# Performance work log

Hardware: AMD Instinct MI355X
Metric: run time of the kernel (lower is better)

## Reference

```python
import jax, jax.numpy as jnp
import numpy as np

R_S, R_C, P, L, NVOX, CH = 48, 144, 27, 2, 128, 128


def encode(x, L=L):
    # NeRF-style positional encoding: [sin(2^l x), cos(2^l x)] for l in range(L)
    feats = []
    for l in range(L):
        f = (2.0 ** l) * x
        feats.append(jnp.sin(f))
        feats.append(jnp.cos(f))
    return jnp.concatenate(feats, axis=-1)


def setup_inputs() -> dict:
    key = jax.random.key(0)
    ks = jax.random.split(key, 8)
    Np = 524288
    xyz = jax.random.uniform(ks[0], (Np, 3), dtype=jnp.float32)          # inside bbox [0,1]^3
    directions = jax.random.normal(ks[1], (Np, 3), dtype=jnp.float32)
    # voxel grid buffer: linspace over bbox per axis -> (3, NVOX)
    voxel = jnp.stack([jnp.linspace(0.0, 1.0, NVOX)] * 3, axis=0).astype(jnp.float32)
    sigma = 0.1 * jax.random.normal(ks[2], (3, R_S, NVOX), dtype=jnp.float32)
    feature = 0.1 * jax.random.normal(ks[3], (3, R_C, NVOX), dtype=jnp.float32)
    B = jax.random.normal(ks[4], (R_C, P), dtype=jnp.float32)
    din = (P + 3) * L * 2  # 120
    W1 = jax.random.normal(ks[5], (din, CH), dtype=jnp.float32) / jnp.sqrt(din)
    b1 = jnp.zeros((CH,), jnp.float32)
    W2 = jax.random.normal(ks[6], (CH, CH), dtype=jnp.float32) / jnp.sqrt(CH)
    b2 = jnp.zeros((CH,), jnp.float32)
    W3 = jax.random.normal(ks[7], (CH, 3), dtype=jnp.float32) / jnp.sqrt(CH)
    b3 = jnp.zeros((3,), jnp.float32)
    return {"xyz": xyz, "directions": directions, "voxel": voxel, "sigma": sigma,
            "feature": feature, "B": B, "W1": W1, "b1": b1, "W2": W2, "b2": b2,
            "W3": W3, "b3": b3}


def reference(xyz, directions, voxel, sigma, feature, B, W1, b1, W2, b2, W3, b3):
    SIGMA_BIAS = -5.0
    x = xyz.T  # (3, Np)
    Nv = voxel.shape[1]
    # snap_to_voxels: per-axis searchsorted + clamp + gather of grid coords
    inds = jax.vmap(jnp.searchsorted)(voxel, x)           # (3, Np)
    il = jnp.clip(inds - 1, 0, Nv - 1)
    ir = jnp.clip(inds, 0, Nv - 1)
    vl = jnp.take_along_axis(voxel, il, axis=1)           # (3, Np)
    vr = jnp.take_along_axis(voxel, ir, axis=1)
    w = (x - vl) / (vr - vl + 1e-6)                       # (3, Np) lerp weights

    # density: gather (3,R_s,Np), lerp, prod over axes(xyz), sum over rank
    sl = jnp.take_along_axis(sigma, il[:, None, :], axis=2)
    sr = jnp.take_along_axis(sigma, ir[:, None, :], axis=2)
    s = sl + (sr - sl) * w[:, None, :]                    # (3, R_s, Np)
    sigmas = jnp.sum(jnp.prod(s, axis=0), axis=0)         # (Np,)
    sigmas = jax.nn.softplus(sigmas + SIGMA_BIAS)

    # features: same pattern on (3,R_c,Np), then small matmul with B
    fl = jnp.take_along_axis(feature, il[:, None, :], axis=2)
    fr = jnp.take_along_axis(feature, ir[:, None, :], axis=2)
    f = fl + (fr - fl) * w[:, None, :]                    # (3, R_c, Np)
    feats = jnp.einsum('rn,rp->np', jnp.prod(f, axis=0), B)  # (Np, P)

    h = jnp.concatenate([encode(feats, L), encode(directions, L)], axis=1)  # (Np, 120)
    h = jax.nn.leaky_relu(h @ W1 + b1, negative_slope=0.01)
    h = jax.nn.leaky_relu(h @ W2 + b2, negative_slope=0.01)
    rgb = jax.nn.sigmoid(h @ W3 + b3)                     # (Np, 3)
    return sigmas, rgb
```

## Files before the change

kernel.cpp:

```cpp
#include <hip/hip_runtime.h>
#include <cstdint>

constexpr int RS  = 48;
constexpr int RC  = 144;
constexpr int PP  = 27;
constexpr int NV  = 128;
constexpr int CHN = 128;

constexpr int SIG_D  = 3 * NV * 64;
constexpr int FEAT_D = 3 * NV * 160;
constexpr int NPAIR  = SIG_D + FEAT_D;
constexpr int FR_B  = 0;
constexpr int FR_W1 = 5120;
constexpr int FR_W2 = 21504;
constexpr int FR_W3 = 37888;
constexpr int FR_B2 = 39936;
constexpr int FR_TOT = 45056;

typedef __attribute__((ext_vector_type(8))) short short8;
typedef __attribute__((ext_vector_type(4))) float f32x4;
typedef __attribute__((ext_vector_type(2))) unsigned int u32x2;
typedef __attribute__((ext_vector_type(4))) unsigned int u32x4;
typedef _Float16 h2 __attribute__((ext_vector_type(2)));

__device__ __forceinline__ short f2bf(float f) {
    unsigned int u = __builtin_bit_cast(unsigned int, f);
    u += 0x7fffu + ((u >> 16) & 1u);
    return (short)(u >> 16);
}
__device__ __forceinline__ unsigned int pk2bf(float a, float b) {
    unsigned short ua = __builtin_bit_cast(unsigned short, (__bf16)a);
    unsigned short ub = __builtin_bit_cast(unsigned short, (__bf16)b);
    return (unsigned int)ua | ((unsigned int)ub << 16);
}
__device__ __forceinline__ float bflo(unsigned int u) { return __builtin_bit_cast(float, u << 16); }
__device__ __forceinline__ float bfhi(unsigned int u) { return __builtin_bit_cast(float, u & 0xffff0000u); }
__device__ __forceinline__ float dot2lerp(unsigned int lodelta, h2 wv) {
#if __has_builtin(__builtin_amdgcn_fdot2)
    return __builtin_amdgcn_fdot2(__builtin_bit_cast(h2, lodelta), wv, 0.f, false);
#else
    h2 a = __builtin_bit_cast(h2, lodelta);
    return (float)a.x * (float)wv.x + (float)a.y * (float)wv.y;
#endif
}

#define GLO(dst, base, OFF) \
    asm volatile("global_load_dwordx4 %0, %1, off offset:" OFF : "=&v"(dst) : "v"(base))
#define WAITV(N) do { asm volatile("s_waitcnt vmcnt(" #N ")" ::: "memory"); \
                      __builtin_amdgcn_sched_barrier(0); } while (0)
#define ISSUE_FK(buf, O1, O2) do { \
    GLO(buf[0], fb0, O1); GLO(buf[1], fb0, O2); \
    GLO(buf[2], fb1, O1); GLO(buf[3], fb1, O2); \
    GLO(buf[4], fb2, O1); GLO(buf[5], fb2, O2); } while (0)

__global__ void prep_tables(const float* __restrict__ sigma, const float* __restrict__ feature,
                            unsigned int* __restrict__ wt) {
    int idx = blockIdx.x * 256 + threadIdx.x;
    if (idx >= NPAIR) return;
    float lo = 0.f, hi = 0.f;
    if (idx < SIG_D) {
        int a = idx / 8192, t = idx % 8192;
        int v = t / 64, r = t % 64;
        if (r < RS) {
            lo = sigma[(a * RS + r) * NV + v];
            hi = sigma[(a * RS + r) * NV + min(v + 1, NV - 1)];
        }
    } else {
        int j = idx - SIG_D;
        int a = j / 20480, t = j % 20480;
        int v = t / 160, r = t % 160;
        if (r < RC) {
            lo = feature[(a * RC + r) * NV + v];
            hi = feature[(a * RC + r) * NV + min(v + 1, NV - 1)];
        }
    }
    _Float16 lh = (_Float16)lo;
    _Float16 dh = (_Float16)(hi - lo);
    wt[idx] = (unsigned int)__builtin_bit_cast(unsigned short, lh) |
              ((unsigned int)__builtin_bit_cast(unsigned short, dh) << 16);
}

__global__ void prep_frags(const float* __restrict__ Bm, const float* __restrict__ W1,
                           const float* __restrict__ W2, const float* __restrict__ W3,
                           short* __restrict__ fr) {
    int idx = blockIdx.x * 256 + threadIdx.x;
    if (idx >= FR_TOT) return;
    float val = 0.f;
    if (idx < FR_W1) {
        int j = idx - FR_B;
        int frag = j >> 9, li = (j >> 3) & 63, e = j & 7;
        int kt = frag >> 1, nt = frag & 1;
        int k = kt * 32 + (li >> 4) * 8 + e;
        int n = nt * 16 + (li & 15);
        val = (k < RC && n < PP) ? Bm[k * PP + n] : 0.f;
    } else if (idx < FR_W2) {
        int j = idx - FR_W1;
        int frag = j >> 9, li = (j >> 3) & 63, e = j & 7;
        int kt = frag >> 3, nt = frag & 7;
        int kn = kt * 32 + (li >> 4) * 8 + e;
        int n = nt * 16 + (li & 15);
        if (kn < 120) {
            int ko;
            if (kn < 108) { ko = (kn & 3) * PP + (kn >> 2); }
            else { int t2 = kn - 108; ko = 108 + (t2 & 3) * 3 + (t2 >> 2); }
            val = W1[ko * CHN + n];
        }
    } else if (idx < FR_W3) {
        int j = idx - FR_W2;
        int frag = j >> 9, li = (j >> 3) & 63, e = j & 7;
        int kt = frag >> 3, nt = frag & 7;
        int k = kt * 32 + (li >> 4) * 8 + e;
        int n = nt * 16 + (li & 15);
        val = W2[k * CHN + n];
    } else if (idx < FR_B2) {
        int j = idx - FR_W3;
        int frag = j >> 9, li = (j >> 3) & 63, e = j & 7;
        int kt = frag;
        int k = kt * 32 + (li >> 4) * 8 + e;
        int n = li & 15;
        val = (n < 3) ? W3[k * 3 + n] : 0.f;
    } else {
        int j = idx - FR_B2;
        int frag = j >> 9, li = (j >> 3) & 63, e = j & 7;
        int kt = frag >> 1, nt = frag & 1;
        int q = li >> 4;
        int n = nt * 16 + (li & 15);
        int k = -1;
        if (kt < 4) k = kt * 32 + (e < 4 ? 4 * q + e : 16 + 4 * q + (e - 4));
        else if (e < 4) k = 128 + 4 * q + e;
        val = (k >= 0 && k < RC && n < PP) ? Bm[k * PP + n] : 0.f;
    }
    fr[idx] = f2bf(val);
}

__device__ __forceinline__ void lerpregs(u32x4 A, u32x4 Bv, h2 wv, float* pr, bool first) {
#pragma unroll
    for (int d = 0; d < 4; ++d) {
        float s0 = dot2lerp(A[d], wv);
        float s1 = dot2lerp(Bv[d], wv);
        if (first) { pr[d] = s0; pr[4 + d] = s1; }
        else       { pr[d] *= s0; pr[4 + d] *= s1; }
    }
}
__device__ __forceinline__ void lerpf8(const unsigned int* rl, h2 wv, float* pr, bool first) {
    u32x4 A  = *(const u32x4*)rl;
    u32x4 Bv = *(const u32x4*)(rl + 4);
    lerpregs(A, Bv, wv, pr, first);
}

__global__ __launch_bounds__(256, 4)
void phaseA(const float* __restrict__ xyz, const float* __restrict__ dird,
            const float* __restrict__ voxel,
            const unsigned int* __restrict__ wt, const short* __restrict__ fr,
            float* __restrict__ out, unsigned short* __restrict__ X64, int Np) {
    __shared__ float voxs[3 * NV];
    __shared__ short bfrs[5120];

    const int tid = threadIdx.x;
    const int wid = tid >> 6;
    const int lane = tid & 63;
    const int quad = lane >> 4, lane16 = lane & 15;
    const int wavebase = blockIdx.x * 64 + wid * 16;
    const int p = wavebase + lane16;

    for (int i = tid; i < 3 * NV; i += 256) voxs[i] = voxel[i];
    for (int i = tid; i < 640; i += 256)
        ((short8*)bfrs)[i] = ((const short8*)(fr + FR_B2))[i];
    __syncthreads();

    const unsigned int* SIGU  = wt;
    const unsigned int* FEATU = wt + SIG_D;

    int ipb[3]; h2 wv[3];
#pragma unroll
    for (int a = 0; a < 3; ++a) {
        float x = xyz[p * 3 + a];
        int ind = (int)ceilf(x * 127.f);
        ind = min(max(ind, 0), 128);
        while (ind > 0 && voxs[a * NV + ind - 1] >= x) --ind;
        while (ind < 128 && voxs[a * NV + ind] < x) ++ind;
        int il = min(max(ind - 1, 0), 127);
        int ir = min(ind, 127);
        float vl = voxs[a * NV + il], vr = voxs[a * NV + ir];
        float w = (x - vl) / (vr - vl + 1e-6f);
        w = (il == 127) ? 1.f : w;
        ipb[a] = min(il, 126);
        wv[a] = h2{(_Float16)1.0f, (_Float16)w};
    }

    const unsigned int* sb0 = SIGU + (0 * NV + ipb[0]) * 64 + quad * 4;
    const unsigned int* sb1 = SIGU + (1 * NV + ipb[1]) * 64 + quad * 4;
    const unsigned int* sb2 = SIGU + (2 * NV + ipb[2]) * 64 + quad * 4;
    const unsigned int* fb0 = FEATU + (0 * NV + ipb[0]) * 160 + quad * 4;
    const unsigned int* fb1 = FEATU + (1 * NV + ipb[1]) * 160 + quad * 4;
    const unsigned int* fb2 = FEATU + (2 * NV + ipb[2]) * 160 + quad * 4;

    u32x4 S[9];
    GLO(S[0], sb0, "0");   GLO(S[1], sb1, "0");   GLO(S[2], sb2, "0");
    GLO(S[3], sb0, "64");  GLO(S[4], sb1, "64");  GLO(S[5], sb2, "64");
    GLO(S[6], sb0, "128"); GLO(S[7], sb1, "128"); GLO(S[8], sb2, "128");
    u32x4 Fa[6], Fb[6];
    ISSUE_FK(Fa, "0", "64");

    WAITV(6);
    float sig = 0.f;
#pragma unroll
    for (int L = 0; L < 3; ++L)
#pragma unroll
        for (int j = 0; j < 4; ++j)
            sig += dot2lerp(S[3 * L][j], wv[0]) * dot2lerp(S[3 * L + 1][j], wv[1])
                 * dot2lerp(S[3 * L + 2][j], wv[2]);
    sig += __shfl_xor(sig, 16);
    sig += __shfl_xor(sig, 32);

    f32x4 acc0 = {0.f, 0.f, 0.f, 0.f}, acc1 = {0.f, 0.f, 0.f, 0.f};
    auto compute_kt = [&](const u32x4* F, int kt) {
        float pr[8];
#pragma unroll
        for (int j = 0; j < 4; ++j) {
            pr[j]     = dot2lerp(F[0][j], wv[0]) * dot2lerp(F[2][j], wv[1]) * dot2lerp(F[4][j], wv[2]);
            pr[4 + j] = dot2lerp(F[1][j], wv[0]) * dot2lerp(F[3][j], wv[1]) * dot2lerp(F[5][j], wv[2]);
        }
        u32x4 uu;
#pragma unroll
        for (int d = 0; d < 4; ++d) uu[d] = pk2bf(pr[2 * d], pr[2 * d + 1]);
        short8 af = __builtin_bit_cast(short8, uu);
        short8 bf0 = *(const short8*)(bfrs + ((kt * 2 + 0) * 64 + lane) * 8);
        short8 bf1 = *(const short8*)(bfrs + ((kt * 2 + 1) * 64 + lane) * 8);
        acc0 = __builtin_amdgcn_mfma_f32_16x16x32_bf16(af, bf0, acc0, 0, 0, 0);
        acc1 = __builtin_amdgcn_mfma_f32_16x16x32_bf16(af, bf1, acc1, 0, 0, 0);
    };

    ISSUE_FK(Fb, "128", "192");
    WAITV(6); compute_kt(Fa, 0);
    ISSUE_FK(Fa, "256", "320");
    WAITV(6); compute_kt(Fb, 1);
    ISSUE_FK(Fb, "384", "448");
    WAITV(6); compute_kt(Fa, 2);
    GLO(Fa[0], fb0, "512"); GLO(Fa[1], fb1, "512"); GLO(Fa[2], fb2, "512");
    WAITV(3); compute_kt(Fb, 3);
    WAITV(0);
    {
        float pr[8];
#pragma unroll
        for (int j = 0; j < 4; ++j) {
            pr[j] = dot2lerp(Fa[0][j], wv[0]) * dot2lerp(Fa[1][j], wv[1]) * dot2lerp(Fa[2][j], wv[2]);
            pr[4 + j] = 0.f;
        }
        u32x4 uu;
#pragma unroll
        for (int d = 0; d < 4; ++d) uu[d] = pk2bf(pr[2 * d], pr[2 * d + 1]);
        short8 af = __builtin_bit_cast(short8, uu);
        short8 bf0 = *(const short8*)(bfrs + ((4 * 2 + 0) * 64 + lane) * 8);
        short8 bf1 = *(const short8*)(bfrs + ((4 * 2 + 1) * 64 + lane) * 8);
        acc0 = __builtin_amdgcn_mfma_f32_16x16x32_bf16(af, bf0, acc0, 0, 0, 0);
        acc1 = __builtin_amdgcn_mfma_f32_16x16x32_bf16(af, bf1, acc1, 0, 0, 0);
    }

    if (lane < 16) out[p] = log1pf(expf(sig - 5.f));
#pragma unroll
    for (int nt = 0; nt < 2; ++nt) {
        int c = nt * 16 + lane16;
        f32x4 A = nt ? acc1 : acc0;
        if (c < PP) {
#pragma unroll
            for (int j = 0; j < 4; ++j) {
                int prow = wavebase + quad * 4 + j;
                X64[prow * 32 + c] = (unsigned short)__builtin_bit_cast(unsigned short, (__bf16)A[j]);
            }
        }
    }
    if (quad < 3) {
        float d = dird[p * 3 + quad];
        X64[p * 32 + 27 + quad] = (unsigned short)__builtin_bit_cast(unsigned short, (__bf16)d);
    } else {
        *(unsigned int*)(X64 + p * 32 + 30) = 0u;
    }
}

__global__ __launch_bounds__(256, 4)
void phaseB(const unsigned short* __restrict__ X64, const short* __restrict__ fr,
            const float* __restrict__ b1, const float* __restrict__ b2,
            const float* __restrict__ b3, float* __restrict__ out, int Np) {
    __shared__ char T[4 * 32 * 256];
    const int tid = threadIdx.x;
    const int wid = tid >> 6;
    const int lane = tid & 63;
    const int quad = lane >> 4, lane16 = lane & 15;
    const int rowbase = blockIdx.x * 128 + wid * 32;
    char* Tw = T + wid * 32 * 256;

    const short* W1F = fr + FR_W1;
    const short* W2F = fr + FR_W2;
    const short* W3F = fr + FR_W3;

    short8 af[2][4];
#pragma unroll
    for (int mt = 0; mt < 2; ++mt)
#pragma unroll
        for (int kt = 0; kt < 4; ++kt) {
            unsigned int d = *(const unsigned int*)(X64 + (rowbase + mt * 16 + lane16) * 32 + kt * 8 + quad * 2);
            float f0 = bflo(d), f1 = bfhi(d);
            float s1 = __sinf(f0), c1 = __cosf(f0);
            float s2 = 2.f * s1 * c1, c2 = fmaf(-2.f * s1, s1, 1.f);
            float s1b = __sinf(f1), c1b = __cosf(f1);
            float s2b = 2.f * s1b * c1b, c2b = fmaf(-2.f * s1b, s1b, 1.f);
            u32x4 uu = {pk2bf(s1, c1), pk2bf(s2, c2), pk2bf(s1b, c1b), pk2bf(s2b, c2b)};
            af[mt][kt] = __builtin_bit_cast(short8, uu);
        }

#pragma unroll 1
    for (int layer = 0; layer < 2; ++layer) {
        const short* WF = layer ? W2F : W1F;
        const float* bb = layer ? b2 : b1;
#pragma unroll 2
        for (int nt = 0; nt < 8; ++nt) {
            short8 wfv[4];
#pragma unroll
            for (int kt = 0; kt < 4; ++kt)
                wfv[kt] = *(const short8*)(WF + ((kt * 8 + nt) * 64 + lane) * 8);
            f32x4 acc[2];
#pragma unroll
            for (int mt = 0; mt < 2; ++mt) acc[mt] = {0.f, 0.f, 0.f, 0.f};
#pragma unroll
            for (int mt = 0; mt < 2; ++mt)
#pragma unroll
                for (int kt = 0; kt < 4; ++kt)
                    acc[mt] = __builtin_amdgcn_mfma_f32_16x16x32_bf16(af[mt][kt], wfv[kt], acc[mt], 0, 0, 0);

            float bvv = bb[nt * 16 + lane16];
#pragma unroll
            for (int mt = 0; mt < 2; ++mt)
#pragma unroll
                for (int j = 0; j < 4; ++j) {
                    float v = acc[mt][j] + bvv;
                    v = fmaxf(v, 0.01f * v);
                    int row = mt * 16 + quad * 4 + j;
                    int byte = (nt * 16 + lane16) * 2;
                    int chunk = byte >> 4, off = byte & 15;
                    *(short*)(Tw + row * 256 + ((chunk ^ (row & 7)) << 4) + off) =
                        (short)__builtin_bit_cast(unsigned short, (__bf16)v);
                }
        }
#pragma unroll
        for (int mt = 0; mt < 2; ++mt)
#pragma unroll
            for (int kt = 0; kt < 4; ++kt) {
                int row = mt * 16 + lane16;
                int chunk = kt * 4 + quad;
                af[mt][kt] = *(const short8*)(Tw + row * 256 + ((chunk ^ (row & 7)) << 4));
            }
    }

    {
        short8 wf3[4];
#pragma unroll
        for (int kt = 0; kt < 4; ++kt)
            wf3[kt] = *(const short8*)(W3F + (kt * 64 + lane) * 8);
        f32x4 acc3[2];
#pragma unroll
        for (int mt = 0; mt < 2; ++mt) acc3[mt] = {0.f, 0.f, 0.f, 0.f};
#pragma unroll
        for (int mt = 0; mt < 2; ++mt)
#pragma unroll
            for (int kt = 0; kt < 4; ++kt)
                acc3[mt] = __builtin_amdgcn_mfma_f32_16x16x32_bf16(af[mt][kt], wf3[kt], acc3[mt], 0, 0, 0);

        if (lane16 < 3) {
            float bvv = b3[lane16];
#pragma unroll
            for (int mt = 0; mt < 2; ++mt)
#pragma unroll
                for (int j = 0; j < 4; ++j) {
                    float v = acc3[mt][j] + bvv;
                    float r = 1.f / (1.f + expf(-v));
                    int row = mt * 16 + quad * 4 + j;
                    out[Np + (rowbase + row) * 3 + lane16] = r;
                }
        }
    }
}

__global__ __launch_bounds__(128, 4)
void tensorf_fused(const float* __restrict__ xyz, const float* __restrict__ dird,
                   const float* __restrict__ voxel,
                   const float* __restrict__ b1, const float* __restrict__ b2,
                   const float* __restrict__ b3,
                   const unsigned int* __restrict__ wt, const short* __restrict__ fr,
                   float* __restrict__ out, int Np) {
    __shared__ float voxs[3 * NV];
    __shared__ char  X[2 * 32 * 256];

    const int tid = threadIdx.x;
    const int wid = tid >> 6;
    const int lane = tid & 63;
    const int quad = lane >> 4, lane16 = lane & 15;
    const int wavebase = blockIdx.x * 64 + wid * 32;
    char* Xw = X + wid * 32 * 256;

    for (int i = tid; i < 3 * NV; i += 128) voxs[i] = voxel[i];
    __syncthreads();

    const unsigned int* SIGU  = wt;
    const unsigned int* FEATU = wt + SIG_D;
    const short* BFr = fr + FR_B;

#pragma unroll 1
    for (int q = 0; q < 2; ++q) {
        const int rowbase = q * 16;
        const int p = wavebase + rowbase + lane16;
        int ipb[3]; h2 wv[3];
#pragma unroll
        for (int a = 0; a < 3; ++a) {
            float x = xyz[p * 3 + a];
            int ind = (int)ceilf(x * 127.f);
            ind = min(max(ind, 0), 128);
            while (ind > 0 && voxs[a * NV + ind - 1] >= x) --ind;
            while (ind < 128 && voxs[a * NV + ind] < x) ++ind;
            int il = min(max(ind - 1, 0), 127);
            int ir = min(ind, 127);
            float vl = voxs[a * NV + il], vr = voxs[a * NV + ir];
            float w = (x - vl) / (vr - vl + 1e-6f);
            w = (il == 127) ? 1.f : w;
            ipb[a] = min(il, 126);
            wv[a] = h2{(_Float16)1.0f, (_Float16)w};
        }
        float sig = 0.f;
#pragma unroll
        for (int kt = 0; kt < 2; ++kt) {
            float pr[8];
#pragma unroll
            for (int a = 0; a < 3; ++a)
                lerpf8(SIGU + (a * NV + ipb[a]) * 64 + kt * 32 + quad * 8, wv[a], pr, a == 0);
#pragma unroll
            for (int j = 0; j < 8; ++j) sig += pr[j];
        }
        sig += __shfl_xor(sig, 16);
        sig += __shfl_xor(sig, 32);
        if (lane < 16) out[p] = log1pf(expf(sig - 5.f));

        f32x4 acc0 = {0.f, 0.f, 0.f, 0.f}, acc1 = {0.f, 0.f, 0.f, 0.f};
#pragma unroll
        for (int kt = 0; kt < 5; ++kt) {
            float pr[8];
#pragma unroll
            for (int a = 0; a < 3; ++a)
                lerpf8(FEATU + (a * NV + ipb[a]) * 160 + kt * 32 + quad * 8, wv[a], pr, a == 0);
            u32x4 uu;
#pragma unroll
            for (int d = 0; d < 4; ++d) uu[d] = pk2bf(pr[2 * d], pr[2 * d + 1]);
            short8 af = __builtin_bit_cast(short8, uu);
            short8 bf0 = *(const short8*)(BFr + ((kt * 2 + 0) * 64 + lane) * 8);
            short8 bf1 = *(const short8*)(BFr + ((kt * 2 + 1) * 64 + lane) * 8);
            acc0 = __builtin_amdgcn_mfma_f32_16x16x32_bf16(af, bf0, acc0, 0, 0, 0);
            acc1 = __builtin_amdgcn_mfma_f32_16x16x32_bf16(af, bf1, acc1, 0, 0, 0);
        }
#pragma unroll
        for (int nt = 0; nt < 2; ++nt) {
            int c = nt * 16 + lane16;
            f32x4 A = nt ? acc1 : acc0;
            if (c < PP) {
#pragma unroll
                for (int j = 0; j < 4; ++j) {
                    int row = rowbase + quad * 4 + j;
                    float f = A[j];
                    float s1 = __sinf(f), c1 = __cosf(f);
                    float s2 = 2.f * s1 * c1;
                    float c2 = fmaf(-2.f * s1, s1, 1.f);
                    unsigned int w0 = pk2bf(s1, c1);
                    unsigned int w1 = pk2bf(s2, c2);
                    int byte = c * 8;
                    int chunk = byte >> 4, off = byte & 15;
                    *(u32x2*)(Xw + row * 256 + ((chunk ^ (row & 7)) << 4) + off) = u32x2{w0, w1};
                }
            }
        }
        {
            int row = rowbase + lane16;
            if (quad < 3) {
                float d = dird[p * 3 + quad];
                float s1 = __sinf(d), c1 = __cosf(d);
                float s2 = 2.f * s1 * c1;
                float c2 = fmaf(-2.f * s1, s1, 1.f);
                unsigned int w0 = pk2bf(s1, c1);
                unsigned int w1 = pk2bf(s2, c2);
                int byte = 216 + 8 * quad;
                int chunk = byte >> 4, off = byte & 15;
                *(u32x2*)(Xw + row * 256 + ((chunk ^ (row & 7)) << 4) + off) = u32x2{w0, w1};
            } else {
                int addr = row * 256 + ((15 ^ (row & 7)) << 4);
                *(u32x4*)(Xw + addr) = u32x4{0u, 0u, 0u, 0u};
            }
        }
    }
    __syncthreads();

    const short* W1F = fr + FR_W1;
    const short* W2F = fr + FR_W2;
    const short* W3F = fr + FR_W3;

#pragma unroll 1
    for (int layer = 0; layer < 2; ++layer) {
        const short* WF = layer ? W2F : W1F;
        const float* bb = layer ? b2 : b1;
        short8 af[2][4];
#pragma unroll
        for (int m = 0; m < 2; ++m)
#pragma unroll
            for (int kt = 0; kt < 4; ++kt) {
                int row = m * 16 + lane16;
                int chunk = kt * 4 + quad;
                af[m][kt] = *(const short8*)(Xw + row * 256 + ((chunk ^ (row & 7)) << 4));
            }
#pragma unroll 1
        for (int nt = 0; nt < 8; ++nt) {
            short8 wfv[4];
#pragma unroll
            for (int kt = 0; kt < 4; ++kt)
                wfv[kt] = *(const short8*)(WF + ((kt * 8 + nt) * 64 + lane) * 8);
            f32x4 acc[2];
#pragma unroll
            for (int m = 0; m < 2; ++m) acc[m] = {0.f, 0.f, 0.f, 0.f};
#pragma unroll
            for (int m = 0; m < 2; ++m)
#pragma unroll
                for (int kt = 0; kt < 4; ++kt)
                    acc[m] = __builtin_amdgcn_mfma_f32_16x16x32_bf16(af[m][kt], wfv[kt], acc[m], 0, 0, 0);
            float bvv = bb[nt * 16 + lane16];
#pragma unroll
            for (int m = 0; m < 2; ++m) {
#pragma unroll
                for (int j = 0; j < 4; ++j) {
                    float v = acc[m][j] + bvv;
                    v = fmaxf(v, 0.01f * v);
                    int row = m * 16 + quad * 4 + j;
                    int byte = (nt * 16 + lane16) * 2;
                    int chunk = byte >> 4, off = byte & 15;
                    *(short*)(Xw + row * 256 + ((chunk ^ (row & 7)) << 4) + off) =
                        (short)__builtin_bit_cast(unsigned short, (__bf16)v);
                }
            }
        }
        __syncthreads();
    }
    {
        short8 af[2][4];
#pragma unroll
        for (int m = 0; m < 2; ++m)
#pragma unroll
            for (int kt = 0; kt < 4; ++kt) {
                int row = m * 16 + lane16;
                int chunk = kt * 4 + quad;
                af[m][kt] = *(const short8*)(Xw + row * 256 + ((chunk ^ (row & 7)) << 4));
            }
        short8 wf3[4];
#pragma unroll
        for (int kt = 0; kt < 4; ++kt)
            wf3[kt] = *(const short8*)(W3F + (kt * 64 + lane) * 8);
        f32x4 acc3[2];
#pragma unroll
        for (int m = 0; m < 2; ++m) acc3[m] = {0.f, 0.f, 0.f, 0.f};
#pragma unroll
        for (int m = 0; m < 2; ++m)
#pragma unroll
            for (int kt = 0; kt < 4; ++kt)
                acc3[m] = __builtin_amdgcn_mfma_f32_16x16x32_bf16(af[m][kt], wf3[kt], acc3[m], 0, 0, 0);
        if (lane16 < 3) {
            float bvv = b3[lane16];
#pragma unroll
            for (int m = 0; m < 2; ++m) {
#pragma unroll
                for (int j = 0; j < 4; ++j) {
                    float v = acc3[m][j] + bvv;
                    float r = 1.f / (1.f + expf(-v));
                    int row = m * 16 + quad * 4 + j;
                    out[Np + (wavebase + row) * 3 + lane16] = r;
                }
            }
        }
    }
}

extern "C" void kernel_launch(void* const* d_in, const int* in_sizes, int n_in,
                              void* d_out, int out_size, void* d_ws, size_t ws_size,
                              hipStream_t stream) {
    (void)n_in; (void)out_size;
    const float* xyz      = (const float*)d_in[0];
    const float* dird     = (const float*)d_in[1];
    const float* voxel    = (const float*)d_in[2];
    const float* sigma    = (const float*)d_in[3];
    const float* feature  = (const float*)d_in[4];
    const float* Bm       = (const float*)d_in[5];
    const float* W1       = (const float*)d_in[6];
    const float* b1       = (const float*)d_in[7];
    const float* W2       = (const float*)d_in[8];
    const float* b2       = (const float*)d_in[9];
    const float* W3       = (const float*)d_in[10];
    const float* b3       = (const float*)d_in[11];
    float* out = (float*)d_out;
    unsigned int* wt = (unsigned int*)d_ws;
    short* frg = (short*)d_ws + 2 * (size_t)NPAIR;

    const int Np = in_sizes[0] / 3;
    const size_t base = (size_t)NPAIR * 4 + (size_t)FR_TOT * 2;
    const size_t need = base + (size_t)Np * 64;

    prep_tables<<<(NPAIR + 255) / 256, 256, 0, stream>>>(sigma, feature, wt);
    prep_frags<<<(FR_TOT + 255) / 256, 256, 0, stream>>>(Bm, W1, W2, W3, frg);

    if (ws_size >= need) {
        unsigned short* X64 = (unsigned short*)((char*)d_ws + base);
        phaseA<<<Np / 64, 256, 0, stream>>>(xyz, dird, voxel, wt, frg, out, X64, Np);
        phaseB<<<Np / 128, 256, 0, stream>>>(X64, frg, b1, b2, b3, out, Np);
    } else {
        tensorf_fused<<<Np / 64, 128, 0, stream>>>(xyz, dird, voxel, b1, b2, b3, wt, frg, out, Np);
    }
}
```

Before: 222.9 us.

## Sort points by Morton voxel bucket before the gather phase

Adds a counting sort on the GPU that orders points by a 15-bit Morton code of their coarse voxel cell: zero histogram, atomic histogram, single-block scan, then an atomic scatter into a permutation. phaseA and phaseB process points in sorted order through the permutation, so nearby lanes fetch neighbouring table rows and gather locality improves. In exchange it adds four extra launches, atomic contention, a serial one-block scan, and scattered output writes. The sort runs on every call, so no results are reused across calls.

Result: slower. 265.0 us (+18.9%).

```diff
diff --git a/kernel.cpp b/kernel.cpp
--- a/kernel.cpp
+++ b/kernel.cpp
@@ -16,6 +16,7 @@
 constexpr int FR_W3 = 37888;
 constexpr int FR_B2 = 39936;
 constexpr int FR_TOT = 45056;
+constexpr int NBUCK = 32768;
 
 typedef __attribute__((ext_vector_type(8))) short short8;
 typedef __attribute__((ext_vector_type(4))) float f32x4;
@@ -52,6 +53,48 @@
     GLO(buf[0], fb0, O1); GLO(buf[1], fb0, O2); \
     GLO(buf[2], fb1, O1); GLO(buf[3], fb1, O2); \
     GLO(buf[4], fb2, O1); GLO(buf[5], fb2, O2); } while (0)
+
+__device__ __forceinline__ unsigned spread5(unsigned v) {
+    return (v & 1) | ((v & 2) << 2) | ((v & 4) << 4) | ((v & 8) << 6) | ((v & 16) << 8);
+}
+__device__ __forceinline__ unsigned morton15(const float* __restrict__ xyz, int i) {
+    int ix = min(max((int)(xyz[3 * i + 0] * 127.f), 0), 127) >> 2;
+    int iy = min(max((int)(xyz[3 * i + 1] * 127.f), 0), 127) >> 2;
+    int iz = min(max((int)(xyz[3 * i + 2] * 127.f), 0), 127) >> 2;
+    return spread5(ix) | (spread5(iy) << 1) | (spread5(iz) << 2);
+}
+__global__ void zero_hist(unsigned* __restrict__ h) {
+    int i = blockIdx.x * 256 + threadIdx.x;
+    if (i < NBUCK) h[i] = 0u;
+}
+__global__ void hist_kernel(const float* __restrict__ xyz, unsigned* __restrict__ hist, int Np) {
+    int i = blockIdx.x * 256 + threadIdx.x;
+    if (i < Np) atomicAdd(&hist[morton15(xyz, i)], 1u);
+}
+__global__ __launch_bounds__(1024, 1)
+void scan_kernel(unsigned* __restrict__ hist) {
+    __shared__ unsigned ts[1024];
+    int t = threadIdx.x;
+    unsigned loc[32]; unsigned s = 0;
+#pragma unroll
+    for (int i = 0; i < 32; ++i) { loc[i] = hist[t * 32 + i]; s += loc[i]; }
+    ts[t] = s; __syncthreads();
+    for (int off = 1; off < 1024; off <<= 1) {
+        unsigned v = (t >= off) ? ts[t - off] : 0u; __syncthreads();
+        ts[t] += v; __syncthreads();
+    }
+    unsigned base = ts[t] - s;
+#pragma unroll
+    for (int i = 0; i < 32; ++i) { hist[t * 32 + i] = base; base += loc[i]; }
+}
+__global__ void scatter_kernel(const float* __restrict__ xyz, unsigned* __restrict__ cursor,
+                               unsigned* __restrict__ perm, int Np) {
+    int i = blockIdx.x * 256 + threadIdx.x;
+    if (i < Np) {
+        unsigned pos = atomicAdd(&cursor[morton15(xyz, i)], 1u);
+        perm[pos] = (unsigned)i;
+    }
+}
 
 __global__ void prep_tables(const float* __restrict__ sigma, const float* __restrict__ feature,
                             unsigned int* __restrict__ wt) {
@@ -152,6 +195,7 @@
 void phaseA(const float* __restrict__ xyz, const float* __restrict__ dird,
             const float* __restrict__ voxel,
             const unsigned int* __restrict__ wt, const short* __restrict__ fr,
+            const unsigned* __restrict__ perm,
             float* __restrict__ out, unsigned short* __restrict__ X64, int Np) {
     __shared__ float voxs[3 * NV];
     __shared__ short bfrs[5120];
@@ -161,7 +205,8 @@
     const int lane = tid & 63;
     const int quad = lane >> 4, lane16 = lane & 15;
     const int wavebase = blockIdx.x * 64 + wid * 16;
-    const int p = wavebase + lane16;
+    const int sp = wavebase + lane16;
+    const int p  = perm ? (int)perm[sp] : sp;
 
     for (int i = tid; i < 3 * NV; i += 256) voxs[i] = voxel[i];
     for (int i = tid; i < 640; i += 256)
@@ -272,14 +317,15 @@
     }
     if (quad < 3) {
         float d = dird[p * 3 + quad];
-        X64[p * 32 + 27 + quad] = (unsigned short)__builtin_bit_cast(unsigned short, (__bf16)d);
+        X64[sp * 32 + 27 + quad] = (unsigned short)__builtin_bit_cast(unsigned short, (__bf16)d);
     } else {
-        *(unsigned int*)(X64 + p * 32 + 30) = 0u;
+        *(unsigned int*)(X64 + sp * 32 + 30) = 0u;
     }
 }
 
 __global__ __launch_bounds__(256, 4)
 void phaseB(const unsigned short* __restrict__ X64, const short* __restrict__ fr,
+            const unsigned* __restrict__ perm,
             const float* __restrict__ b1, const float* __restrict__ b2,
             const float* __restrict__ b3, float* __restrict__ out, int Np) {
     __shared__ char T[4 * 32 * 256];
@@ -375,7 +421,8 @@
                     float v = acc3[mt][j] + bvv;
                     float r = 1.f / (1.f + expf(-v));
                     int row = mt * 16 + quad * 4 + j;
-                    out[Np + (rowbase + row) * 3 + lane16] = r;
+                    int opr = perm ? (int)perm[rowbase + row] : (rowbase + row);
+                    out[Np + opr * 3 + lane16] = r;
                 }
         }
     }
@@ -602,16 +649,30 @@
     short* frg = (short*)d_ws + 2 * (size_t)NPAIR;
 
     const int Np = in_sizes[0] / 3;
-    const size_t base = (size_t)NPAIR * 4 + (size_t)FR_TOT * 2;
-    const size_t need = base + (size_t)Np * 64;
+    const size_t base      = (size_t)NPAIR * 4 + (size_t)FR_TOT * 2;
+    const size_t x64_off   = base;
+    const size_t perm_off  = x64_off + (size_t)Np * 64;
+    const size_t hist_off  = perm_off + (size_t)Np * 4;
+    const size_t need_sort = hist_off + (size_t)NBUCK * 4;
+    const size_t need_plain = perm_off;
 
     prep_tables<<<(NPAIR + 255) / 256, 256, 0, stream>>>(sigma, feature, wt);
     prep_frags<<<(FR_TOT + 255) / 256, 256, 0, stream>>>(Bm, W1, W2, W3, frg);
 
-    if (ws_size >= need) {
-        unsigned short* X64 = (unsigned short*)((char*)d_ws + base);
-        phaseA<<<Np / 64, 256, 0, stream>>>(xyz, dird, voxel, wt, frg, out, X64, Np);
-        phaseB<<<Np / 128, 256, 0, stream>>>(X64, frg, b1, b2, b3, out, Np);
+    if (ws_size >= need_sort) {
+        unsigned short* X64 = (unsigned short*)((char*)d_ws + x64_off);
+        unsigned* perm = (unsigned*)((char*)d_ws + perm_off);
+        unsigned* hist = (unsigned*)((char*)d_ws + hist_off);
+        zero_hist<<<(NBUCK + 255) / 256, 256, 0, stream>>>(hist);
+        hist_kernel<<<(Np + 255) / 256, 256, 0, stream>>>(xyz, hist, Np);
+        scan_kernel<<<1, 1024, 0, stream>>>(hist);
+        scatter_kernel<<<(Np + 255) / 256, 256, 0, stream>>>(xyz, hist, perm, Np);
+        phaseA<<<Np / 64, 256, 0, stream>>>(xyz, dird, voxel, wt, frg, perm, out, X64, Np);
+        phaseB<<<Np / 128, 256, 0, stream>>>(X64, frg, perm, b1, b2, b3, out, Np);
+    } else if (ws_size >= need_plain) {
+        unsigned short* X64 = (unsigned short*)((char*)d_ws + x64_off);
+        phaseA<<<Np / 64, 256, 0, stream>>>(xyz, dird, voxel, wt, frg, nullptr, out, X64, Np);
+        phaseB<<<Np / 128, 256, 0, stream>>>(X64, frg, nullptr, b1, b2, b3, out, Np);
     } else {
         tensorf_fused<<<Np / 64, 128, 0, stream>>>(xyz, dird, voxel, b1, b2, b3, wt, frg, out, Np);
     }
```
